# Optimization experiments

Hardware: AMD Instinct MI355X
Metric: run time of the kernel (lower is better)

Reference implementation:

```python
import jax, jax.numpy as jnp
import numpy as np

B, C_IN, C_OUT, N, M = 64, 64, 64, 8192, 64


def setup_inputs() -> dict:
    key = jax.random.key(0)
    k1, k2, k3 = jax.random.split(key, 3)
    init_std = np.sqrt(2.0 / C_IN).astype(np.float32)
    v = jax.random.normal(k1, (B, C_IN, N), dtype=jnp.float32)
    w_real = jax.random.normal(k2, (C_IN, C_OUT, M), dtype=jnp.float32) * init_std
    w_imag = jax.random.normal(k3, (C_IN, C_OUT, M), dtype=jnp.float32) * init_std
    return {"v": v, "w_real": w_real, "w_imag": w_imag}


def reference(v, w_real, w_imag):
    # v: [B, C_in, N] real; weights: [C_in, C_out, M] complex (real/imag parts)
    n = v.shape[-1]
    m = w_real.shape[-1]
    W = w_real + 1j * w_imag                       # [C_in, C_out, M] complex64
    v_hat = jnp.fft.rfft(v, axis=-1)               # [B, C_in, N//2+1]
    v_hat_trunc = v_hat[..., :m]                   # keep low-frequency modes
    out_hat = jnp.einsum('biM,ioM->boM', v_hat_trunc, W)  # mode mixing
    n_freq = n // 2 + 1
    pad = n_freq - m
    out_hat_padded = jnp.pad(out_hat, ((0, 0), (0, 0), (0, pad)))  # zero high modes
    out = jnp.fft.irfft(out_hat_padded, n=n, axis=-1)  # [B, C_out, N] real
    return out
```

## Files before the change

kernel.cpp:

```cpp
#include <hip/hip_runtime.h>
#include <hip/hip_bf16.h>
#include <hip/hip_fp16.h>

#define NN 8192
#define NROWS 4096
#define KSPLIT 8
#define KCHUNK (NN / KSPLIT)
static constexpr float TWO_PI = 6.28318530717958647692f;

typedef __attribute__((ext_vector_type(8))) _Float16 half8;
typedef __attribute__((ext_vector_type(4))) float floatx4;

__global__ __launch_bounds__(256) void gen_fwd(_Float16* __restrict__ bt) {
    const int idx = blockIdx.x * 256 + threadIdx.x;
    const int j = idx >> 13;
    const int k = idx & (NN - 1);
    const int m = j & 63;
    const int t = (m * k) & (NN - 1);
    float s, c;
    sincosf((float)t * (TWO_PI / (float)NN), &s, &c);
    bt[idx] = (_Float16)((j < 64) ? c : -s);
}

__global__ __launch_bounds__(256) void gen_inv(_Float16* __restrict__ gt) {
    const int idx = blockIdx.x * 256 + threadIdx.x;
    const int n = idx >> 7;
    const int c = idx & 127;
    const int m = c & 63;
    const int t = (m * n) & (NN - 1);
    float s, cc;
    sincosf((float)t * (TWO_PI / (float)NN), &s, &cc);
    gt[idx] = (_Float16)((c < 64) ? cc : s);
}

static __device__ inline half8 cvt8(float4 a, float4 b) {
    half8 h;
    h[0] = (_Float16)a.x; h[1] = (_Float16)a.y; h[2] = (_Float16)a.z; h[3] = (_Float16)a.w;
    h[4] = (_Float16)b.x; h[5] = (_Float16)b.y; h[6] = (_Float16)b.z; h[7] = (_Float16)b.w;
    return h;
}

__global__ __launch_bounds__(256) void gemm_fwd(const float* __restrict__ v,
                                                const _Float16* __restrict__ bt,
                                                float* __restrict__ part) {
    const int wid   = threadIdx.x >> 6;
    const int lane  = threadIdx.x & 63;
    const int l15   = lane & 15;
    const int g     = lane >> 4;
    const int mtile = blockIdx.x >> 3;
    const int s     = blockIdx.x & (KSPLIT - 1);

    const int rowA = mtile * 64 + wid * 16 + l15;
    const int k0   = s * KCHUNK + g * 8;
    const float*    ap = v + (size_t)rowA * NN + k0;
    const _Float16* bp = bt + k0 + (size_t)l15 * NN;

    floatx4 acc[8] = {};
    for (int kk = 0; kk < KCHUNK; kk += 32) {
        float4 a0 = *(const float4*)(ap + kk);
        float4 a1 = *(const float4*)(ap + kk + 4);
        half8 af = cvt8(a0, a1);
        #pragma unroll
        for (int jt = 0; jt < 8; ++jt) {
            half8 bf = *(const half8*)(bp + (size_t)jt * 16 * NN + kk);
            acc[jt] = __builtin_amdgcn_mfma_f32_16x16x32_f16(af, bf, acc[jt], 0, 0, 0);
        }
    }

    float* pout = part + (size_t)s * NROWS * 128;
    const int prow = mtile * 64 + wid * 16 + g * 4;
    #pragma unroll
    for (int jt = 0; jt < 8; ++jt)
        #pragma unroll
        for (int r = 0; r < 4; ++r)
            pout[(size_t)(prow + r) * 128 + jt * 16 + l15] = acc[jt][r];
}

__global__ __launch_bounds__(256) void reduce_part(const float* __restrict__ part,
                                                   float* __restrict__ vhat) {
    const int idx = blockIdx.x * 256 + threadIdx.x;
    float a = 0.f;
    #pragma unroll
    for (int s = 0; s < KSPLIT; ++s) a += part[(size_t)s * NROWS * 128 + idx];
    vhat[idx] = a;
}

__global__ __launch_bounds__(256) void mix(const float* __restrict__ vhat,
                                           const float* __restrict__ wr,
                                           const float* __restrict__ wi,
                                           _Float16* __restrict__ xc) {
    const int m  = threadIdx.x & 63;
    const int ol = threadIdx.x >> 6;
    const int b  = blockIdx.x >> 4;
    const int o  = ((blockIdx.x & 15) << 2) + ol;

    float ar = 0.f, ai = 0.f;
    #pragma unroll 4
    for (int i = 0; i < 64; ++i) {
        const float* vrow = vhat + (size_t)(b * 64 + i) * 128;
        const float vr = vrow[m];
        const float vi = vrow[64 + m];
        const float wre = wr[((size_t)(i * 64 + o)) * 64 + m];
        const float wim = wi[((size_t)(i * 64 + o)) * 64 + m];
        ar = fmaf(vr, wre, ar);  ar = fmaf(-vi, wim, ar);
        ai = fmaf(vr, wim, ai);  ai = fmaf(vi, wre, ai);
    }
    _Float16* xrow = xc + (size_t)(b * 64 + o) * 128;
    if (m == 0) {
        xrow[0]  = (_Float16)(ar * (1.f / (float)NN));
        xrow[64] = (_Float16)0.f;
    } else {
        xrow[m]      = (_Float16)(ar * (2.f / (float)NN));
        xrow[64 + m] = (_Float16)(-ai * (2.f / (float)NN));
    }
}

__global__ __launch_bounds__(256) void gemm_inv(const _Float16* __restrict__ xc,
                                                const _Float16* __restrict__ gt,
                                                float* __restrict__ out) {
    const int wid  = threadIdx.x >> 6;
    const int lane = threadIdx.x & 63;
    const int l15  = lane & 15;
    const int g    = lane >> 4;
    const int mt   = blockIdx.x >> 5;
    const int nt   = blockIdx.x & 31;
    const int row0 = mt * 16;
    const int col0 = nt * 256 + wid * 64;

    half8 af[4];
    const _Float16* ap = xc + (size_t)(row0 + l15) * 128 + g * 8;
    #pragma unroll
    for (int ks = 0; ks < 4; ++ks) af[ks] = *(const half8*)(ap + ks * 32);

    floatx4 acc[4] = {};
    #pragma unroll
    for (int jt = 0; jt < 4; ++jt) {
        const _Float16* gp = gt + (size_t)(col0 + jt * 16 + l15) * 128 + g * 8;
        #pragma unroll
        for (int ks = 0; ks < 4; ++ks) {
            half8 bf = *(const half8*)(gp + ks * 32);
            acc[jt] = __builtin_amdgcn_mfma_f32_16x16x32_f16(af[ks], bf, acc[jt], 0, 0, 0);
        }
    }

    #pragma unroll
    for (int jt = 0; jt < 4; ++jt)
        #pragma unroll
        for (int r = 0; r < 4; ++r)
            out[(size_t)(row0 + g * 4 + r) * NN + col0 + jt * 16 + l15] = acc[jt][r];
}

extern "C" void kernel_launch(void* const* d_in, const int* in_sizes, int n_in,
                              void* d_out, int out_size, void* d_ws, size_t ws_size,
                              hipStream_t stream) {
    const float* v  = (const float*)d_in[0];
    const float* wr = (const float*)d_in[1];
    const float* wi = (const float*)d_in[2];
    float* out = (float*)d_out;

    char* ws = (char*)d_ws;
    _Float16* btF  = (_Float16*)(ws);
    _Float16* gt   = (_Float16*)(ws + (2u << 20));
    float*    part = (float*)   (ws + (4u << 20));
    float*    vhat = (float*)   (ws + (20u << 20));
    _Float16* xc   = (_Float16*)(ws + (22u << 20));

    gen_fwd<<<4096, 256, 0, stream>>>(btF);
    gen_inv<<<4096, 256, 0, stream>>>(gt);
    gemm_fwd<<<64 * KSPLIT, 256, 0, stream>>>(v, btF, part);
    reduce_part<<<2048, 256, 0, stream>>>(part, vhat);
    mix<<<1024, 256, 0, stream>>>(vhat, wr, wi, xc);
    gemm_inv<<<8192, 256, 0, stream>>>(xc, gt, out);
}
```

Measured before the change: 367.2 us.

## Restructure forward DFT GEMM: 16-row tiles, column split across waves, deeper loads

After: 399.0 us. +8.7%, slower.

```diff
diff --git a/kernel.cpp b/kernel.cpp
--- a/kernel.cpp
+++ b/kernel.cpp
@@ -47,33 +47,42 @@
     const int lane  = threadIdx.x & 63;
     const int l15   = lane & 15;
     const int g     = lane >> 4;
+    const int s     = blockIdx.x & (KSPLIT - 1);
     const int mtile = blockIdx.x >> 3;
-    const int s     = blockIdx.x & (KSPLIT - 1);
 
-    const int rowA = mtile * 64 + wid * 16 + l15;
+    const int rowA = mtile * 16 + l15;
     const int k0   = s * KCHUNK + g * 8;
-    const float*    ap = v + (size_t)rowA * NN + k0;
-    const _Float16* bp = bt + k0 + (size_t)l15 * NN;
+    const float*    ap  = v + (size_t)rowA * NN + k0;
+    const int j0 = wid * 32;
+    const _Float16* bp0 = bt + (size_t)(j0 + l15) * NN + k0;
+    const _Float16* bp1 = bt + (size_t)(j0 + 16 + l15) * NN + k0;
 
-    floatx4 acc[8] = {};
-    for (int kk = 0; kk < KCHUNK; kk += 32) {
-        float4 a0 = *(const float4*)(ap + kk);
-        float4 a1 = *(const float4*)(ap + kk + 4);
-        half8 af = cvt8(a0, a1);
+    floatx4 acc0 = {}, acc1 = {};
+    for (int kk = 0; kk < KCHUNK; kk += 128) {
+        float4 a[8];
+        half8 b0[4], b1[4];
         #pragma unroll
-        for (int jt = 0; jt < 8; ++jt) {
-            half8 bf = *(const half8*)(bp + (size_t)jt * 16 * NN + kk);
-            acc[jt] = __builtin_amdgcn_mfma_f32_16x16x32_f16(af, bf, acc[jt], 0, 0, 0);
+        for (int t = 0; t < 4; ++t) {
+            a[2 * t]     = *(const float4*)(ap + kk + t * 32);
+            a[2 * t + 1] = *(const float4*)(ap + kk + t * 32 + 4);
+            b0[t] = *(const half8*)(bp0 + kk + t * 32);
+            b1[t] = *(const half8*)(bp1 + kk + t * 32);
+        }
+        #pragma unroll
+        for (int t = 0; t < 4; ++t) {
+            half8 af = cvt8(a[2 * t], a[2 * t + 1]);
+            acc0 = __builtin_amdgcn_mfma_f32_16x16x32_f16(af, b0[t], acc0, 0, 0, 0);
+            acc1 = __builtin_amdgcn_mfma_f32_16x16x32_f16(af, b1[t], acc1, 0, 0, 0);
         }
     }
 
-    float* pout = part + (size_t)s * NROWS * 128;
-    const int prow = mtile * 64 + wid * 16 + g * 4;
+    float* pout = part + (size_t)s * NROWS * 128
+                + (size_t)(mtile * 16 + g * 4) * 128 + j0 + l15;
     #pragma unroll
-    for (int jt = 0; jt < 8; ++jt)
-        #pragma unroll
-        for (int r = 0; r < 4; ++r)
-            pout[(size_t)(prow + r) * 128 + jt * 16 + l15] = acc[jt][r];
+    for (int r = 0; r < 4; ++r) {
+        pout[(size_t)r * 128]      = acc0[r];
+        pout[(size_t)r * 128 + 16] = acc1[r];
+    }
 }
 
 __global__ __launch_bounds__(256) void reduce_part(const float* __restrict__ part,
@@ -167,7 +176,7 @@
 
     gen_fwd<<<4096, 256, 0, stream>>>(btF);
     gen_inv<<<4096, 256, 0, stream>>>(gt);
-    gemm_fwd<<<64 * KSPLIT, 256, 0, stream>>>(v, btF, part);
+    gemm_fwd<<<256 * KSPLIT, 256, 0, stream>>>(v, btF, part);
     reduce_part<<<2048, 256, 0, stream>>>(part, vhat);
     mix<<<1024, 256, 0, stream>>>(vhat, wr, wi, xc);
     gemm_inv<<<8192, 256, 0, stream>>>(xc, gt, out);
```

## Stage forward GEMM tiles through LDS with async loads; reuse DFT basis in inverse GEMM

Applied to the files above, without the earlier changes.

Result: faster. 298.8 us (-18.6%).

```diff
diff --git a/kernel.cpp b/kernel.cpp
--- a/kernel.cpp
+++ b/kernel.cpp
@@ -1,15 +1,24 @@
 #include <hip/hip_runtime.h>
 #include <hip/hip_bf16.h>
 #include <hip/hip_fp16.h>
+#include <stdint.h>
 
 #define NN 8192
 #define NROWS 4096
 #define KSPLIT 8
 #define KCHUNK (NN / KSPLIT)
+#define BM 128
+#define BK 64
+#define NPH (KCHUNK / BK)
 static constexpr float TWO_PI = 6.28318530717958647692f;
 
 typedef __attribute__((ext_vector_type(8))) _Float16 half8;
 typedef __attribute__((ext_vector_type(4))) float floatx4;
+
+#define GLD_LDS(gsrc, ldst)                                                           \
+    __builtin_amdgcn_global_load_lds(                                                 \
+        (const __attribute__((address_space(1))) uint32_t*)(gsrc),                    \
+        (__attribute__((address_space(3))) uint32_t*)(ldst), 16, 0, 0)
 
 __global__ __launch_bounds__(256) void gen_fwd(_Float16* __restrict__ bt) {
     const int idx = blockIdx.x * 256 + threadIdx.x;
@@ -40,40 +49,79 @@
     return h;
 }
 
-__global__ __launch_bounds__(256) void gemm_fwd(const float* __restrict__ v,
-                                                const _Float16* __restrict__ bt,
-                                                float* __restrict__ part) {
-    const int wid   = threadIdx.x >> 6;
-    const int lane  = threadIdx.x & 63;
-    const int l15   = lane & 15;
-    const int g     = lane >> 4;
+__global__ __launch_bounds__(512, 2) void gemm_fwd(const float* __restrict__ v,
+                                                   const _Float16* __restrict__ bt,
+                                                   float* __restrict__ part) {
+    __shared__ float    lA[2][BM * BK];
+    __shared__ _Float16 lB[2][BM * BK];
+    const int tid  = threadIdx.x;
+    const int w    = tid >> 6;
+    const int lane = tid & 63;
+    const int l15  = lane & 15;
+    const int g    = lane >> 4;
+    const int s     = blockIdx.x & (KSPLIT - 1);
     const int mtile = blockIdx.x >> 3;
-    const int s     = blockIdx.x & (KSPLIT - 1);
-
-    const int rowA = mtile * 64 + wid * 16 + l15;
-    const int k0   = s * KCHUNK + g * 8;
-    const float*    ap = v + (size_t)rowA * NN + k0;
-    const _Float16* bp = bt + k0 + (size_t)l15 * NN;
+    const int kbase = s * KCHUNK;
+
+    const int rA = lane >> 4, cA = lane & 15;
+    const int rB = lane >> 3, cB = lane & 7;
+
+#define STAGE(buf, t)                                                                  \
+    {                                                                                  \
+        const int kk_ = kbase + (t) * BK;                                              \
+        _Pragma("unroll")                                                              \
+        for (int i_ = 0; i_ < 4; ++i_) {                                               \
+            const int row_ = w * 16 + i_ * 4 + rA;                                     \
+            GLD_LDS(v + (size_t)(mtile * BM + row_) * NN + kk_                         \
+                      + ((cA ^ (row_ & 7)) << 2),                                      \
+                    &lA[buf][(w * 16 + i_ * 4) * BK]);                                 \
+        }                                                                              \
+        _Pragma("unroll")                                                              \
+        for (int i_ = 0; i_ < 2; ++i_) {                                               \
+            const int row_ = w * 16 + i_ * 8 + rB;                                     \
+            GLD_LDS(bt + (size_t)row_ * NN + kk_ + ((cB ^ (row_ & 7)) << 3),           \
+                    &lB[buf][(w * 16 + i_ * 8) * BK]);                                 \
+        }                                                                              \
+    }
 
     floatx4 acc[8] = {};
-    for (int kk = 0; kk < KCHUNK; kk += 32) {
-        float4 a0 = *(const float4*)(ap + kk);
-        float4 a1 = *(const float4*)(ap + kk + 4);
-        half8 af = cvt8(a0, a1);
-        #pragma unroll
-        for (int jt = 0; jt < 8; ++jt) {
-            half8 bf = *(const half8*)(bp + (size_t)jt * 16 * NN + kk);
-            acc[jt] = __builtin_amdgcn_mfma_f32_16x16x32_f16(af, bf, acc[jt], 0, 0, 0);
-        }
-    }
-
-    float* pout = part + (size_t)s * NROWS * 128;
-    const int prow = mtile * 64 + wid * 16 + g * 4;
+    const int hh = l15 & 7;
+
+    STAGE(0, 0)
+    for (int t = 0; t < NPH; ++t) {
+        if (t + 1 < NPH) {
+            STAGE((t + 1) & 1, t + 1)
+            asm volatile("s_waitcnt vmcnt(6)" ::: "memory");
+        } else {
+            asm volatile("s_waitcnt vmcnt(0)" ::: "memory");
+        }
+        __builtin_amdgcn_s_barrier();
+        const float*    la = lA[t & 1];
+        const _Float16* lb = lB[t & 1];
+        #pragma unroll
+        for (int ks = 0; ks < 2; ++ks) {
+            const int ga = ks * 8 + g * 2;
+            float4 x0 = *(const float4*)&la[(w * 16 + l15) * BK + (((ga)     ^ hh) << 2)];
+            float4 x1 = *(const float4*)&la[(w * 16 + l15) * BK + (((ga + 1) ^ hh) << 2)];
+            half8 af = cvt8(x0, x1);
+            #pragma unroll
+            for (int jt = 0; jt < 8; ++jt) {
+                half8 bf = *(const half8*)&lb[(jt * 16 + l15) * BK
+                                              + (((ks * 4 + g) ^ hh) << 3)];
+                acc[jt] = __builtin_amdgcn_mfma_f32_16x16x32_f16(af, bf, acc[jt], 0, 0, 0);
+            }
+        }
+        __builtin_amdgcn_s_barrier();
+    }
+#undef STAGE
+
+    float* pout = part + (size_t)s * NROWS * 128
+                + (size_t)(mtile * BM + w * 16 + g * 4) * 128 + l15;
     #pragma unroll
     for (int jt = 0; jt < 8; ++jt)
         #pragma unroll
         for (int r = 0; r < 4; ++r)
-            pout[(size_t)(prow + r) * 128 + jt * 16 + l15] = acc[jt][r];
+            pout[(size_t)r * 128 + jt * 16] = acc[jt][r];
 }
 
 __global__ __launch_bounds__(256) void reduce_part(const float* __restrict__ part,
@@ -115,39 +163,47 @@
     }
 }
 
-__global__ __launch_bounds__(256) void gemm_inv(const _Float16* __restrict__ xc,
-                                                const _Float16* __restrict__ gt,
-                                                float* __restrict__ out) {
-    const int wid  = threadIdx.x >> 6;
+__global__ __launch_bounds__(512, 4) void gemm_inv(const _Float16* __restrict__ xc,
+                                                   const _Float16* __restrict__ gt,
+                                                   float* __restrict__ out) {
+    const int w    = threadIdx.x >> 6;
     const int lane = threadIdx.x & 63;
     const int l15  = lane & 15;
     const int g    = lane >> 4;
     const int mt   = blockIdx.x >> 5;
     const int nt   = blockIdx.x & 31;
-    const int row0 = mt * 16;
-    const int col0 = nt * 256 + wid * 64;
-
-    half8 af[4];
-    const _Float16* ap = xc + (size_t)(row0 + l15) * 128 + g * 8;
+    const int col0 = nt * 256 + w * 32;
+
+    half8 bf[2][4];
     #pragma unroll
-    for (int ks = 0; ks < 4; ++ks) af[ks] = *(const half8*)(ap + ks * 32);
-
-    floatx4 acc[4] = {};
-    #pragma unroll
-    for (int jt = 0; jt < 4; ++jt) {
-        const _Float16* gp = gt + (size_t)(col0 + jt * 16 + l15) * 128 + g * 8;
+    for (int jt = 0; jt < 2; ++jt)
+        #pragma unroll
+        for (int ks = 0; ks < 4; ++ks)
+            bf[jt][ks] = *(const half8*)(gt + (size_t)(col0 + jt * 16 + l15) * 128
+                                            + ks * 32 + g * 8);
+
+    #pragma unroll 2
+    for (int rc = 0; rc < 16; ++rc) {
+        const int row0 = mt * 256 + rc * 16;
+        const _Float16* ap = xc + (size_t)(row0 + l15) * 128 + g * 8;
+        half8 af[4];
+        #pragma unroll
+        for (int ks = 0; ks < 4; ++ks) af[ks] = *(const half8*)(ap + ks * 32);
+
+        floatx4 a0 = {}, a1 = {};
         #pragma unroll
         for (int ks = 0; ks < 4; ++ks) {
-            half8 bf = *(const half8*)(gp + ks * 32);
-            acc[jt] = __builtin_amdgcn_mfma_f32_16x16x32_f16(af[ks], bf, acc[jt], 0, 0, 0);
-        }
-    }
-
-    #pragma unroll
-    for (int jt = 0; jt < 4; ++jt)
-        #pragma unroll
-        for (int r = 0; r < 4; ++r)
-            out[(size_t)(row0 + g * 4 + r) * NN + col0 + jt * 16 + l15] = acc[jt][r];
+            a0 = __builtin_amdgcn_mfma_f32_16x16x32_f16(af[ks], bf[0][ks], a0, 0, 0, 0);
+            a1 = __builtin_amdgcn_mfma_f32_16x16x32_f16(af[ks], bf[1][ks], a1, 0, 0, 0);
+        }
+
+        float* op = out + (size_t)(row0 + g * 4) * NN + col0 + l15;
+        #pragma unroll
+        for (int r = 0; r < 4; ++r) {
+            op[(size_t)r * NN]      = a0[r];
+            op[(size_t)r * NN + 16] = a1[r];
+        }
+    }
 }
 
 extern "C" void kernel_launch(void* const* d_in, const int* in_sizes, int n_in,
@@ -167,8 +223,8 @@
 
     gen_fwd<<<4096, 256, 0, stream>>>(btF);
     gen_inv<<<4096, 256, 0, stream>>>(gt);
-    gemm_fwd<<<64 * KSPLIT, 256, 0, stream>>>(v, btF, part);
+    gemm_fwd<<<32 * KSPLIT, 512, 0, stream>>>(v, btF, part);
     reduce_part<<<2048, 256, 0, stream>>>(part, vhat);
     mix<<<1024, 256, 0, stream>>>(vhat, wr, wi, xc);
-    gemm_inv<<<8192, 256, 0, stream>>>(xc, gt, out);
-}
+    gemm_inv<<<512, 512, 0, stream>>>(xc, gt, out);
+}
```
